# Optimization experiments

Measured on AMD Instinct MI355X. Metric: run time of the kernel, lower is better.

The kernel has to match this reference:

```python
import jax, jax.numpy as jnp
import numpy as np


def setup_inputs() -> dict:
    key = jax.random.key(0)
    k1, k2, k3 = jax.random.split(key, 3)
    B, NF, Fm, H, NC = 4, 4096, 32, 128, 256
    x = jax.random.normal(k1, (B, NF, Fm, H), dtype=jnp.float32)
    segment_ids = jax.random.randint(k2, (NF,), 0, NC)  # fine -> coarse assignment
    W = jax.random.normal(k3, (1, H), dtype=jnp.float32) / np.sqrt(H)  # Linear(H, 1) weight
    b = jnp.zeros((1,), dtype=jnp.float32)                              # Linear(H, 1) bias
    return {"x": x, "W": W, "b": b, "segment_ids": segment_ids, "num_coarse": NC}


def reference(x, W, b, segment_ids, num_coarse):
    # x: [B, NF, Fm, H]; scores = Linear(mean over Fm) -> [B, NF]
    scores = jnp.einsum('bnh,h->bn', x.mean(axis=2), W[0]) + b[0]

    def per_batch(s, xi):
        # segmented stable softmax over fine nodes within each coarse group
        smax = jax.ops.segment_max(s, segment_ids, num_segments=num_coarse)
        e = jnp.exp(s - smax[segment_ids])
        denom = jax.ops.segment_sum(e, segment_ids, num_segments=num_coarse)
        w = e / denom[segment_ids]                      # [NF]
        # score-weighted scatter-reduce into coarse nodes: [NC, Fm, H]
        return jax.ops.segment_sum(w[:, None, None] * xi, segment_ids,
                                   num_segments=num_coarse)

    return jax.vmap(per_batch)(scores, x)  # [B, NC, Fm, H]
```

## Files before the change

### kernel.cpp

```cpp
#include <hip/hip_runtime.h>
#include <math.h>

#define B   4
#define NF  4096
#define FM  32
#define H   128
#define NC  256
#define ROW (FM * H)
#define RQ  (ROW / 4)
#define MAXM 1024

__global__ __launch_bounds__(256) void k_csr(const int* __restrict__ seg,
                                             int* __restrict__ offs,
                                             int* __restrict__ perm) {
    __shared__ int cnt[NC], sc[NC], cursor[NC];
    const int t = threadIdx.x;

    cnt[t] = 0;
    __syncthreads();
#pragma unroll
    for (int i = 0; i < NF / 256; ++i)
        atomicAdd(&cnt[seg[t + i * 256]], 1);
    __syncthreads();

    sc[t] = cnt[t];
    __syncthreads();
    for (int d = 1; d < NC; d <<= 1) {
        int v = (t >= d) ? sc[t - d] : 0;
        __syncthreads();
        sc[t] += v;
        __syncthreads();
    }
    const int ex = sc[t] - cnt[t];
    offs[t]   = ex;
    cursor[t] = ex;
    if (t == 0) offs[NC] = NF;
    __syncthreads();

#pragma unroll
    for (int i = 0; i < NF / 256; ++i) {
        const int n = t + i * 256;
        perm[atomicAdd(&cursor[seg[n]], 1)] = n;
    }
}

__global__ __launch_bounds__(256) void k_fused(const float* __restrict__ x,
                                               const float* __restrict__ W,
                                               const float* __restrict__ bias,
                                               const int* __restrict__ offs,
                                               const int* __restrict__ perm,
                                               float* __restrict__ out) {
    __shared__ float red[8];
    __shared__ int   list[MAXM];

    const int t    = threadIdx.x;
    const int wid  = t >> 6;
    const int lane = t & 63;
    const int c    = blockIdx.x & (NC - 1);
    const int b    = blockIdx.x >> 8;

    const int off0 = offs[c];
    const int m    = offs[c + 1] - off0;

    for (int k = t; k < m && k < MAXM; k += 256)
        list[k] = perm[off0 + k];
    __syncthreads();

    const float4 w4     = ((const float4*)W)[t & 31];
    const float  inv_fm = 1.0f / FM;
    const float  b0     = bias[0];
    const float4* xb    = (const float4*)x + (size_t)b * NF * RQ;

    float4 acc0 = {0,0,0,0}, acc1 = {0,0,0,0}, acc2 = {0,0,0,0}, acc3 = {0,0,0,0};
    float  mx = -INFINITY, denom = 0.f;

    float4 c0, c1, c2, c3;
    if (m > 0) {
        const float4* rp = xb + (size_t)list[0] * RQ + t;
        c0 = rp[0]; c1 = rp[256]; c2 = rp[512]; c3 = rp[768];
    }

    for (int r = 0; r < m; ++r) {
        float4 n0, n1, n2, n3;
        const bool more = (r + 1 < m);
        if (more) {
            const int nrow = (r + 1 < MAXM) ? list[r + 1] : perm[off0 + r + 1];
            const float4* np = xb + (size_t)nrow * RQ + t;
            n0 = np[0]; n1 = np[256]; n2 = np[512]; n3 = np[768];
        }

        const float sx = c0.x + c1.x + c2.x + c3.x;
        const float sy = c0.y + c1.y + c2.y + c3.y;
        const float sz = c0.z + c1.z + c2.z + c3.z;
        const float sw = c0.w + c1.w + c2.w + c3.w;
        float p = sx * w4.x + sy * w4.y + sz * w4.z + sw * w4.w;
#pragma unroll
        for (int off = 32; off >= 1; off >>= 1)
            p += __shfl_xor(p, off, 64);
        if (lane == 0) red[(r & 1) * 4 + wid] = p;
        __syncthreads();
        const int sl = (r & 1) * 4;
        const float s = (red[sl] + red[sl + 1] + red[sl + 2] + red[sl + 3])
                        * inv_fm + b0;

        if (s > mx) {
            const float scale = __expf(mx - s);
            denom *= scale;
            acc0.x *= scale; acc0.y *= scale; acc0.z *= scale; acc0.w *= scale;
            acc1.x *= scale; acc1.y *= scale; acc1.z *= scale; acc1.w *= scale;
            acc2.x *= scale; acc2.y *= scale; acc2.z *= scale; acc2.w *= scale;
            acc3.x *= scale; acc3.y *= scale; acc3.z *= scale; acc3.w *= scale;
            mx = s;
        }
        const float e = __expf(s - mx);
        denom += e;
        acc0.x += e * c0.x; acc0.y += e * c0.y; acc0.z += e * c0.z; acc0.w += e * c0.w;
        acc1.x += e * c1.x; acc1.y += e * c1.y; acc1.z += e * c1.z; acc1.w += e * c1.w;
        acc2.x += e * c2.x; acc2.y += e * c2.y; acc2.z += e * c2.z; acc2.w += e * c2.w;
        acc3.x += e * c3.x; acc3.y += e * c3.y; acc3.z += e * c3.z; acc3.w += e * c3.w;

        if (more) { c0 = n0; c1 = n1; c2 = n2; c3 = n3; }
    }

    const float inv = (denom > 0.f) ? (1.0f / denom) : 0.f;
    float4* op = (float4*)(out + (size_t)(b * NC + c) * ROW) + t;
    acc0.x *= inv; acc0.y *= inv; acc0.z *= inv; acc0.w *= inv;
    acc1.x *= inv; acc1.y *= inv; acc1.z *= inv; acc1.w *= inv;
    acc2.x *= inv; acc2.y *= inv; acc2.z *= inv; acc2.w *= inv;
    acc3.x *= inv; acc3.y *= inv; acc3.z *= inv; acc3.w *= inv;
    op[0] = acc0; op[256] = acc1; op[512] = acc2; op[768] = acc3;
}

extern "C" void kernel_launch(void* const* d_in, const int* in_sizes, int n_in,
                              void* d_out, int out_size, void* d_ws, size_t ws_size,
                              hipStream_t stream) {
    const float* x    = (const float*)d_in[0];
    const float* W    = (const float*)d_in[1];
    const float* bias = (const float*)d_in[2];
    const int*   seg  = (const int*)d_in[3];
    float*       out  = (float*)d_out;

    int* offs = (int*)d_ws;
    int* perm = offs + (NC + 1);

    k_csr  <<<1,      256, 0, stream>>>(seg, offs, perm);
    k_fused<<<B * NC, 256, 0, stream>>>(x, W, bias, offs, perm, out);
}
```

Before: 66.20 us.

## Fuse CSR build into main kernel and pair large with small segments per block

Removes the separate single-block CSR kernel. Each block now rebuilds the segment histogram and its per-segment member lists in shared memory, which drops one launch and the serial dependency between the two kernels. Segments are ranked by size, and each block handles the pair of rank p and rank 255-p, so the total row count per block is balanced across the grid. In exchange every block redundantly reads the 16KB segment array, does an O(NC) rank computation and runs two block-wide scans, and the grid is halved to 512 blocks, which may lower latency hiding.

```diff
diff --git a/kernel.cpp b/kernel.cpp
--- a/kernel.cpp
+++ b/kernel.cpp
@@ -8,62 +8,58 @@
 #define NC  256
 #define ROW (FM * H)
 #define RQ  (ROW / 4)
-#define MAXM 1024
-
-__global__ __launch_bounds__(256) void k_csr(const int* __restrict__ seg,
-                                             int* __restrict__ offs,
-                                             int* __restrict__ perm) {
-    __shared__ int cnt[NC], sc[NC], cursor[NC];
-    const int t = threadIdx.x;
-
-    cnt[t] = 0;
-    __syncthreads();
-#pragma unroll
-    for (int i = 0; i < NF / 256; ++i)
-        atomicAdd(&cnt[seg[t + i * 256]], 1);
-    __syncthreads();
-
-    sc[t] = cnt[t];
-    __syncthreads();
-    for (int d = 1; d < NC; d <<= 1) {
-        int v = (t >= d) ? sc[t - d] : 0;
-        __syncthreads();
-        sc[t] += v;
-        __syncthreads();
-    }
-    const int ex = sc[t] - cnt[t];
-    offs[t]   = ex;
-    cursor[t] = ex;
-    if (t == 0) offs[NC] = NF;
-    __syncthreads();
-
-#pragma unroll
-    for (int i = 0; i < NF / 256; ++i) {
-        const int n = t + i * 256;
-        perm[atomicAdd(&cursor[seg[n]], 1)] = n;
-    }
-}
 
 __global__ __launch_bounds__(256) void k_fused(const float* __restrict__ x,
                                                const float* __restrict__ W,
                                                const float* __restrict__ bias,
-                                               const int* __restrict__ offs,
-                                               const int* __restrict__ perm,
+                                               const int* __restrict__ seg,
                                                float* __restrict__ out) {
+    __shared__ __align__(16) int cnt[NC];
+    __shared__ int   scn[256];
+    __shared__ int   list[NF];
     __shared__ float red[8];
-    __shared__ int   list[MAXM];
+    __shared__ int   s_c[2];
+    __shared__ int   s_m;
 
     const int t    = threadIdx.x;
     const int wid  = t >> 6;
     const int lane = t & 63;
-    const int c    = blockIdx.x & (NC - 1);
-    const int b    = blockIdx.x >> 8;
+    const int pr   = blockIdx.x >> 2;
+    const int b    = blockIdx.x & 3;
 
-    const int off0 = offs[c];
-    const int m    = offs[c + 1] - off0;
+    int sv[16];
+    cnt[t] = 0;
+    __syncthreads();
+    {
+        const int4* s4 = (const int4*)seg;
+#pragma unroll
+        for (int k = 0; k < 4; ++k) {
+            int4 v = s4[t * 4 + k];
+            sv[k * 4 + 0] = v.x; sv[k * 4 + 1] = v.y;
+            sv[k * 4 + 2] = v.z; sv[k * 4 + 3] = v.w;
+        }
+#pragma unroll
+        for (int k = 0; k < 16; ++k)
+            atomicAdd(&cnt[sv[k]], 1);
+    }
+    __syncthreads();
 
-    for (int k = t; k < m && k < MAXM; k += 256)
-        list[k] = perm[off0 + k];
+    {
+        const int my = cnt[t];
+        int r = 0;
+        const int4* c4 = (const int4*)cnt;
+#pragma unroll
+        for (int j = 0; j < 64; ++j) {
+            const int4 cv = c4[j];
+            const int base = j * 4;
+            r += (cv.x > my) || (cv.x == my && (base + 0) < t);
+            r += (cv.y > my) || (cv.y == my && (base + 1) < t);
+            r += (cv.z > my) || (cv.z == my && (base + 2) < t);
+            r += (cv.w > my) || (cv.w == my && (base + 3) < t);
+        }
+        if (r == pr)       s_c[0] = t;
+        if (r == 255 - pr) s_c[1] = t;
+    }
     __syncthreads();
 
     const float4 w4     = ((const float4*)W)[t & 31];
@@ -71,64 +67,89 @@
     const float  b0     = bias[0];
     const float4* xb    = (const float4*)x + (size_t)b * NF * RQ;
 
-    float4 acc0 = {0,0,0,0}, acc1 = {0,0,0,0}, acc2 = {0,0,0,0}, acc3 = {0,0,0,0};
-    float  mx = -INFINITY, denom = 0.f;
+    for (int half = 0; half < 2; ++half) {
+        const int c = s_c[half];
 
-    float4 c0, c1, c2, c3;
-    if (m > 0) {
-        const float4* rp = xb + (size_t)list[0] * RQ + t;
-        c0 = rp[0]; c1 = rp[256]; c2 = rp[512]; c3 = rp[768];
-    }
+        int loc = 0;
+#pragma unroll
+        for (int k = 0; k < 16; ++k) loc += (sv[k] == c);
+        scn[t] = loc;
+        __syncthreads();
+        for (int d = 1; d < 256; d <<= 1) {
+            int v = (t >= d) ? scn[t - d] : 0;
+            __syncthreads();
+            scn[t] += v;
+            __syncthreads();
+        }
+        if (t == 255) s_m = scn[255];
+        int pos = scn[t] - loc;
+        __syncthreads();
+#pragma unroll
+        for (int k = 0; k < 16; ++k)
+            if (sv[k] == c) list[pos++] = t * 16 + k;
+        __syncthreads();
+        const int m = s_m;
 
-    for (int r = 0; r < m; ++r) {
-        float4 n0, n1, n2, n3;
-        const bool more = (r + 1 < m);
-        if (more) {
-            const int nrow = (r + 1 < MAXM) ? list[r + 1] : perm[off0 + r + 1];
-            const float4* np = xb + (size_t)nrow * RQ + t;
-            n0 = np[0]; n1 = np[256]; n2 = np[512]; n3 = np[768];
+        float4 acc0 = {0,0,0,0}, acc1 = {0,0,0,0};
+        float4 acc2 = {0,0,0,0}, acc3 = {0,0,0,0};
+        float  mx = -INFINITY, denom = 0.f;
+
+        float4 c0, c1, c2, c3;
+        if (m > 0) {
+            const float4* rp = xb + (size_t)list[0] * RQ + t;
+            c0 = rp[0]; c1 = rp[256]; c2 = rp[512]; c3 = rp[768];
         }
 
-        const float sx = c0.x + c1.x + c2.x + c3.x;
-        const float sy = c0.y + c1.y + c2.y + c3.y;
-        const float sz = c0.z + c1.z + c2.z + c3.z;
-        const float sw = c0.w + c1.w + c2.w + c3.w;
-        float p = sx * w4.x + sy * w4.y + sz * w4.z + sw * w4.w;
+        for (int r = 0; r < m; ++r) {
+            float4 n0, n1, n2, n3;
+            const bool more = (r + 1 < m);
+            if (more) {
+                const float4* np = xb + (size_t)list[r + 1] * RQ + t;
+                n0 = np[0]; n1 = np[256]; n2 = np[512]; n3 = np[768];
+            }
+
+            float p = (c0.x + c1.x + c2.x + c3.x) * w4.x
+                    + (c0.y + c1.y + c2.y + c3.y) * w4.y
+                    + (c0.z + c1.z + c2.z + c3.z) * w4.z
+                    + (c0.w + c1.w + c2.w + c3.w) * w4.w;
 #pragma unroll
-        for (int off = 32; off >= 1; off >>= 1)
-            p += __shfl_xor(p, off, 64);
-        if (lane == 0) red[(r & 1) * 4 + wid] = p;
+            for (int off = 32; off >= 1; off >>= 1)
+                p += __shfl_xor(p, off, 64);
+            if (lane == 0) red[(r & 1) * 4 + wid] = p;
+            __syncthreads();
+            const int sl = (r & 1) * 4;
+            const float s = (red[sl] + red[sl+1] + red[sl+2] + red[sl+3])
+                            * inv_fm + b0;
+
+            if (s > mx) {
+                const float scale = __expf(mx - s);
+                denom *= scale;
+                acc0.x *= scale; acc0.y *= scale; acc0.z *= scale; acc0.w *= scale;
+                acc1.x *= scale; acc1.y *= scale; acc1.z *= scale; acc1.w *= scale;
+                acc2.x *= scale; acc2.y *= scale; acc2.z *= scale; acc2.w *= scale;
+                acc3.x *= scale; acc3.y *= scale; acc3.z *= scale; acc3.w *= scale;
+                mx = s;
+            }
+            const float e = __expf(s - mx);
+            denom += e;
+            acc0.x += e * c0.x; acc0.y += e * c0.y; acc0.z += e * c0.z; acc0.w += e * c0.w;
+            acc1.x += e * c1.x; acc1.y += e * c1.y; acc1.z += e * c1.z; acc1.w += e * c1.w;
+            acc2.x += e * c2.x; acc2.y += e * c2.y; acc2.z += e * c2.z; acc2.w += e * c2.w;
+            acc3.x += e * c3.x; acc3.y += e * c3.y; acc3.z += e * c3.z; acc3.w += e * c3.w;
+
+            if (more) { c0 = n0; c1 = n1; c2 = n2; c3 = n3; }
+        }
+
+        const float inv = (denom > 0.f) ? (1.0f / denom) : 0.f;
+        float4* op = (float4*)(out + (size_t)(b * NC + c) * ROW) + t;
+        acc0.x *= inv; acc0.y *= inv; acc0.z *= inv; acc0.w *= inv;
+        acc1.x *= inv; acc1.y *= inv; acc1.z *= inv; acc1.w *= inv;
+        acc2.x *= inv; acc2.y *= inv; acc2.z *= inv; acc2.w *= inv;
+        acc3.x *= inv; acc3.y *= inv; acc3.z *= inv; acc3.w *= inv;
+        op[0] = acc0; op[256] = acc1; op[512] = acc2; op[768] = acc3;
+
         __syncthreads();
-        const int sl = (r & 1) * 4;
-        const float s = (red[sl] + red[sl + 1] + red[sl + 2] + red[sl + 3])
-                        * inv_fm + b0;
-
-        if (s > mx) {
-            const float scale = __expf(mx - s);
-            denom *= scale;
-            acc0.x *= scale; acc0.y *= scale; acc0.z *= scale; acc0.w *= scale;
-            acc1.x *= scale; acc1.y *= scale; acc1.z *= scale; acc1.w *= scale;
-            acc2.x *= scale; acc2.y *= scale; acc2.z *= scale; acc2.w *= scale;
-            acc3.x *= scale; acc3.y *= scale; acc3.z *= scale; acc3.w *= scale;
-            mx = s;
-        }
-        const float e = __expf(s - mx);
-        denom += e;
-        acc0.x += e * c0.x; acc0.y += e * c0.y; acc0.z += e * c0.z; acc0.w += e * c0.w;
-        acc1.x += e * c1.x; acc1.y += e * c1.y; acc1.z += e * c1.z; acc1.w += e * c1.w;
-        acc2.x += e * c2.x; acc2.y += e * c2.y; acc2.z += e * c2.z; acc2.w += e * c2.w;
-        acc3.x += e * c3.x; acc3.y += e * c3.y; acc3.z += e * c3.z; acc3.w += e * c3.w;
-
-        if (more) { c0 = n0; c1 = n1; c2 = n2; c3 = n3; }
     }
-
-    const float inv = (denom > 0.f) ? (1.0f / denom) : 0.f;
-    float4* op = (float4*)(out + (size_t)(b * NC + c) * ROW) + t;
-    acc0.x *= inv; acc0.y *= inv; acc0.z *= inv; acc0.w *= inv;
-    acc1.x *= inv; acc1.y *= inv; acc1.z *= inv; acc1.w *= inv;
-    acc2.x *= inv; acc2.y *= inv; acc2.z *= inv; acc2.w *= inv;
-    acc3.x *= inv; acc3.y *= inv; acc3.z *= inv; acc3.w *= inv;
-    op[0] = acc0; op[256] = acc1; op[512] = acc2; op[768] = acc3;
 }
 
 extern "C" void kernel_launch(void* const* d_in, const int* in_sizes, int n_in,
@@ -140,9 +161,5 @@
     const int*   seg  = (const int*)d_in[3];
     float*       out  = (float*)d_out;
 
-    int* offs = (int*)d_ws;
-    int* perm = offs + (NC + 1);
-
-    k_csr  <<<1,      256, 0, stream>>>(seg, offs, perm);
-    k_fused<<<B * NC, 256, 0, stream>>>(x, W, bias, offs, perm, out);
+    k_fused<<<(NC / 2) * B, 256, 0, stream>>>(x, W, bias, seg, out);
 }
```

Result: faster. 57.93 us (-12.5%).
